# Performance work log

Hardware: AMD Instinct MI355X
Metric: run time of the kernel (lower is better)

## Reference

```python
import jax, jax.numpy as jnp
import numpy as np

B, T, D_IN = 256, 2048, 64
H1, H2, D_OUT = 256, 256, 2


def setup_inputs() -> dict:
    key = jax.random.key(0)
    ks = jax.random.split(key, 12)
    s = lambda fan_in: 1.0 / np.sqrt(fan_in)
    u = lambda k, shape, b: jax.random.uniform(k, shape, jnp.float32, -b, b)
    return {
        "input_tensor": jax.random.normal(ks[0], (B, T, D_IN), jnp.float32),
        # layer 0 LSTMCell params (torch layout: [4H, in], gate order i,f,g,o)
        "W_ih0": u(ks[1], (4 * H1, D_IN), s(H1)),
        "W_hh0": u(ks[2], (4 * H1, H1), s(H1)),
        "b_ih0": u(ks[3], (4 * H1,), s(H1)),
        "b_hh0": u(ks[4], (4 * H1,), s(H1)),
        # layer 1 LSTMCell params
        "W_ih1": u(ks[5], (4 * H2, H1), s(H2)),
        "W_hh1": u(ks[6], (4 * H2, H2), s(H2)),
        "b_ih1": u(ks[7], (4 * H2,), s(H2)),
        "b_hh1": u(ks[8], (4 * H2,), s(H2)),
        # dense head
        "W_dense": u(ks[9], (D_OUT, H2), s(H2)),
        "b_dense": u(ks[10], (D_OUT,), s(H2)),
    }


def _lstm_cell(x, h, c, W_ih, W_hh, b_ih, b_hh):
    # gates: [B, 4H]; torch gate order i, f, g, o
    g = x @ W_ih.T + h @ W_hh.T + (b_ih + b_hh)
    i, f, gg, o = jnp.split(g, 4, axis=-1)
    c_new = jax.nn.sigmoid(f) * c + jax.nn.sigmoid(i) * jnp.tanh(gg)
    h_new = jax.nn.sigmoid(o) * jnp.tanh(c_new)
    return h_new, c_new


def reference(input_tensor, W_ih0, W_hh0, b_ih0, b_hh0,
              W_ih1, W_hh1, b_ih1, b_hh1, W_dense, b_dense):
    b = input_tensor.shape[0]
    h0 = jnp.zeros((b, H1), input_tensor.dtype)
    c0 = jnp.zeros((b, H1), input_tensor.dtype)
    h1 = jnp.zeros((b, H2), input_tensor.dtype)
    c1 = jnp.zeros((b, H2), input_tensor.dtype)

    def step(carry, x_t):
        h0, c0, h1, c1 = carry
        h0, c0 = _lstm_cell(x_t, h0, c0, W_ih0, W_hh0, b_ih0, b_hh0)
        h1, c1 = _lstm_cell(h0, h1, c1, W_ih1, W_hh1, b_ih1, b_hh1)
        return (h0, c0, h1, c1), None

    xs = jnp.swapaxes(input_tensor, 0, 1)  # [T, B, D_IN]
    (h0, c0, h1, c1), _ = jax.lax.scan(step, (h0, c0, h1, c1), xs)
    # dropout_rate=0.0 -> identity; final_act_type='none' -> identity
    out = h1 @ W_dense.T + b_dense  # [B, D_OUT]
    return out
```

## Files before the change

### kernel.cpp

```cpp
#include <hip/hip_runtime.h>
#include <math.h>

#define TT 2048
#define DIN 64
#define HH 256
#define BR 32

typedef __attribute__((ext_vector_type(8))) short bf16x8;
typedef __attribute__((ext_vector_type(4))) float f32x4;
typedef unsigned short u16;

#define XS_STR 72
#define HS_STR 264
#define GB_STR 36

#define OFF_XS_HI  0
#define OFF_XS_LO  (OFF_XS_HI + 32*XS_STR)
#define OFF_HS0_HI (OFF_XS_LO + 32*XS_STR)
#define OFF_HS0_LO (OFF_HS0_HI + 32*HS_STR)
#define OFF_HS1_HI (OFF_HS0_LO + 32*HS_STR)
#define OFF_HS1_LO (OFF_HS1_HI + 32*HS_STR)
#define OFF_W0LO   (OFF_HS1_LO + 32*HS_STR)
#define OFF_W1LO   (OFF_W0LO + 1280*8)
#define SH_SHORTS  (OFF_W1LO + 2048*8)
#define SH_BYTES   (SH_SHORTS*2)
#define LDS_BYTES  (SH_BYTES + 2368*4)

__device__ __forceinline__ u16 f2bf(float f){
    unsigned u = __builtin_bit_cast(unsigned, f);
    u += 0x7fffu + ((u >> 16) & 1u);
    return (u16)(u >> 16);
}
__device__ __forceinline__ float bf2f(u16 h){
    unsigned u = ((unsigned)h) << 16;
    return __builtin_bit_cast(float, u);
}
__device__ __forceinline__ float sigf(float v){ return 1.0f/(1.0f+__expf(-v)); }

__device__ __forceinline__ void group_barrier(unsigned* cnt, unsigned target){
    __syncthreads();
    if (threadIdx.x == 0) {
        __hip_atomic_fetch_add(cnt, 1u, __ATOMIC_RELEASE, __HIP_MEMORY_SCOPE_AGENT);
        while (__hip_atomic_load(cnt, __ATOMIC_ACQUIRE, __HIP_MEMORY_SCOPE_AGENT) < target)
            __builtin_amdgcn_s_sleep(1);
    }
    __syncthreads();
}

__device__ __forceinline__ void split8(float4 a, float4 b, bf16x8& hi, bf16x8& lo){
    float v[8] = {a.x,a.y,a.z,a.w,b.x,b.y,b.z,b.w};
    #pragma unroll
    for (int j=0;j<8;++j){
        u16 h = f2bf(v[j]);
        hi[j] = (short)h;
        lo[j] = (short)f2bf(v[j] - bf2f(h));
    }
}

__global__ __launch_bounds__(256, 1)
void lstm_mfma(const float* __restrict__ x,
               const float* __restrict__ Wih0, const float* __restrict__ Whh0,
               const float* __restrict__ bih0, const float* __restrict__ bhh0,
               const float* __restrict__ Wih1, const float* __restrict__ Whh1,
               const float* __restrict__ bih1, const float* __restrict__ bhh1,
               const float* __restrict__ Wd,   const float* __restrict__ bd,
               float* __restrict__ out, u16* __restrict__ hb,
               unsigned* __restrict__ counters)
{
    extern __shared__ char smem[];
    short* sh  = (short*)smem;
    float* sf  = (float*)(smem + SH_BYTES);
    float* gb0 = sf;
    float* gb1 = sf + 1152;
    float* b0s = sf + 2304;
    float* b1s = sf + 2336;

    const int tid = threadIdx.x;
    const int w   = blockIdx.x;
    const int rb  = w & 7;
    const int ug  = w >> 3;
    const int rbase = rb * BR;
    const int u0  = ug * 8;

    unsigned* cnt = counters + rb * 64;


    const int l  = tid & 63;
    const int wv = tid >> 6;
    const int mt = wv >> 1, nt = wv & 1;
    const int c  = l & 15, ks = l >> 4;
    const int gbx = nt*2 + (c >> 3);
    const int g   = gbx*256 + u0 + (c & 7);

    bf16x8 w0h[10];
    #pragma unroll
    for (int kt = 0; kt < 10; ++kt) {
        int k = kt*32 + ks*8;
        const float* p = (k < 64) ? (Wih0 + (size_t)g*64 + k)
                                  : (Whh0 + (size_t)g*256 + (k - 64));
        bf16x8 hi_, lo_;
        split8(*(const float4*)p, *(const float4*)(p+4), hi_, lo_);
        w0h[kt] = hi_;
    }
    bf16x8 w1h[16];
    #pragma unroll
    for (int kt = 0; kt < 16; ++kt) {
        int k = kt*32 + ks*8;
        const float* p = (k < 256) ? (Wih1 + (size_t)g*256 + k)
                                   : (Whh1 + (size_t)g*256 + (k - 256));
        bf16x8 hi_, lo_;
        split8(*(const float4*)p, *(const float4*)(p+4), hi_, lo_);
        w1h[kt] = hi_;
    }
    for (int f = tid; f < 1280; f += 256) {
        int c_ = f & 15, ks_ = (f>>4)&3, nt_ = (f>>6)&1, kt_ = f>>7;
        int g_ = (nt_*2 + (c_>>3))*256 + u0 + (c_&7);
        int k_ = kt_*32 + ks_*8;
        const float* p = (k_ < 64) ? (Wih0 + (size_t)g_*64 + k_)
                                   : (Whh0 + (size_t)g_*256 + (k_ - 64));
        bf16x8 hi_, lo_;
        split8(*(const float4*)p, *(const float4*)(p+4), hi_, lo_);
        *(bf16x8*)(sh + OFF_W0LO + f*8) = lo_;
    }
    for (int f = tid; f < 2048; f += 256) {
        int c_ = f & 15, ks_ = (f>>4)&3, nt_ = (f>>6)&1, kt_ = f>>7;
        int g_ = (nt_*2 + (c_>>3))*256 + u0 + (c_&7);
        int k_ = kt_*32 + ks_*8;
        const float* p = (k_ < 256) ? (Wih1 + (size_t)g_*256 + k_)
                                    : (Whh1 + (size_t)g_*256 + (k_ - 256));
        bf16x8 hi_, lo_;
        split8(*(const float4*)p, *(const float4*)(p+4), hi_, lo_);
        *(bf16x8*)(sh + OFF_W1LO + f*8) = lo_;
    }

    if (tid < 32) {
        int gg_ = (tid >> 3)*256 + u0 + (tid & 7);
        b0s[tid] = bih0[gg_] + bhh0[gg_];
        b1s[tid] = bih1[gg_] + bhh1[gg_];
    }
    {
        int zr = tid >> 3, zu = tid & 7;
        size_t off = (size_t)(rbase + zr)*HH + u0 + zu;
        hb[off] = 0; hb[65536 + off] = 0;
        hb[131072 + off] = 0; hb[196608 + off] = 0;
        hb[262144 + off] = 0; hb[327680 + off] = 0;
        hb[393216 + off] = 0; hb[458752 + off] = 0;
    }
    {
        int xr = tid >> 3, xk = (tid & 7)*8;
        const float* xp = x + (size_t)(rbase + xr)*(TT*DIN) + xk;
        bf16x8 xh, xl;
        split8(*(const float4*)xp, *(const float4*)(xp+4), xh, xl);
        *(bf16x8*)(sh + OFF_XS_HI + xr*XS_STR + xk) = xh;
        *(bf16x8*)(sh + OFF_XS_LO + xr*XS_STR + xk) = xl;
    }
    unsigned epoch = 1;
    group_barrier(cnt, 32u*epoch);

    const int arow = mt*16 + c;
    const short* axh = sh + OFF_XS_HI  + arow*XS_STR + ks*8;
    const short* axl = sh + OFF_XS_LO  + arow*XS_STR + ks*8;
    const short* a0h = sh + OFF_HS0_HI + arow*HS_STR + ks*8;
    const short* a0l = sh + OFF_HS0_LO + arow*HS_STR + ks*8;
    const short* a1h = sh + OFF_HS1_HI + arow*HS_STR + ks*8;
    const short* a1l = sh + OFF_HS1_LO + arow*HS_STR + ks*8;
    const short* b0lo = sh + OFF_W0LO + (nt*64 + ks*16 + c)*8;
    const short* b1lo = sh + OFF_W1LO + (nt*64 + ks*16 + c)*8;
    float* gw0 = gb0 + (mt*16 + ks*4)*GB_STR + nt*16 + c;
    float* gw1 = gb1 + (mt*16 + ks*4)*GB_STR + nt*16 + c;
    const int ur = tid >> 3, uu = tid & 7;
    const size_t poff = (size_t)(rbase + ur)*HH + u0 + uu;

    float c0s = 0.f, c1s = 0.f;

    for (int k = 0; k <= TT; ++k) {
        {
            const unsigned rdo = ((k + 1) & 1) * 65536u;
            const u16* s0h = hb + rdo;
            const u16* s0l = hb + 131072 + rdo;
            const u16* s1h = hb + 262144 + rdo;
            const u16* s1l = hb + 393216 + rdo;
            #pragma unroll
            for (int j = 0; j < 4; ++j) {
                int cid = tid + j*256;
                int hr = cid >> 5, hk = (cid & 31)*8;
                size_t goff = (size_t)(rbase + hr)*HH + hk;
                int loff = hr*HS_STR + hk;
                *(uint4*)(sh + OFF_HS0_HI + loff) = *(const uint4*)(s0h + goff);
                *(uint4*)(sh + OFF_HS0_LO + loff) = *(const uint4*)(s0l + goff);
                *(uint4*)(sh + OFF_HS1_HI + loff) = *(const uint4*)(s1h + goff);
                *(uint4*)(sh + OFF_HS1_LO + loff) = *(const uint4*)(s1l + goff);
            }
        }
        __syncthreads();

        if (k < TT) {
            f32x4 ac[4] = {};
            #pragma unroll
            for (int kt = 0; kt < 10; ++kt) {
                const short* ph = (kt < 2) ? (axh + kt*32) : (a0h + (kt-2)*32);
                const short* pl = (kt < 2) ? (axl + kt*32) : (a0l + (kt-2)*32);
                bf16x8 ah = *(const bf16x8*)ph;
                bf16x8 al = *(const bf16x8*)pl;
                bf16x8 wl = *(const bf16x8*)(b0lo + kt*1024);
                const int q = kt & 3;
                ac[q] = __builtin_amdgcn_mfma_f32_16x16x32_bf16(ah, w0h[kt], ac[q], 0,0,0);
                ac[q] = __builtin_amdgcn_mfma_f32_16x16x32_bf16(al, w0h[kt], ac[q], 0,0,0);
                ac[q] = __builtin_amdgcn_mfma_f32_16x16x32_bf16(ah, wl,      ac[q], 0,0,0);
            }
            f32x4 aa = (ac[0] + ac[1]) + (ac[2] + ac[3]);
            gw0[0]        = aa[0];
            gw0[GB_STR]   = aa[1];
            gw0[2*GB_STR] = aa[2];
            gw0[3*GB_STR] = aa[3];
        }
        if (k >= 1) {
            f32x4 ac[4] = {};
            #pragma unroll
            for (int kt = 0; kt < 16; ++kt) {
                const short* ph = (kt < 8) ? (a0h + kt*32) : (a1h + (kt-8)*32);
                const short* pl = (kt < 8) ? (a0l + kt*32) : (a1l + (kt-8)*32);
                bf16x8 ah = *(const bf16x8*)ph;
                bf16x8 al = *(const bf16x8*)pl;
                bf16x8 wl = *(const bf16x8*)(b1lo + kt*1024);
                const int q = kt & 3;
                ac[q] = __builtin_amdgcn_mfma_f32_16x16x32_bf16(ah, w1h[kt], ac[q], 0,0,0);
                ac[q] = __builtin_amdgcn_mfma_f32_16x16x32_bf16(al, w1h[kt], ac[q], 0,0,0);
                ac[q] = __builtin_amdgcn_mfma_f32_16x16x32_bf16(ah, wl,      ac[q], 0,0,0);
            }
            f32x4 aa = (ac[0] + ac[1]) + (ac[2] + ac[3]);
            gw1[0]        = aa[0];
            gw1[GB_STR]   = aa[1];
            gw1[2*GB_STR] = aa[2];
            gw1[3*GB_STR] = aa[3];
        }
        __syncthreads();

        const unsigned wro = (k & 1) * 65536u;
        if (k < TT) {
            float gi = gb0[ur*GB_STR + uu]      + b0s[uu];
            float gf = gb0[ur*GB_STR + 8 + uu]  + b0s[8+uu];
            float gg = gb0[ur*GB_STR + 16 + uu] + b0s[16+uu];
            float go = gb0[ur*GB_STR + 24 + uu] + b0s[24+uu];
            c0s = sigf(gf)*c0s + sigf(gi)*tanhf(gg);
            float hn = sigf(go)*tanhf(c0s);
            u16 hh_ = f2bf(hn);
            u16 hl_ = f2bf(hn - bf2f(hh_));
            (hb + wro)[poff]          = hh_;
            (hb + 131072 + wro)[poff] = hl_;
        }
        if (k >= 1) {
            float gi = gb1[ur*GB_STR + uu]      + b1s[uu];
            float gf = gb1[ur*GB_STR + 8 + uu]  + b1s[8+uu];
            float gg = gb1[ur*GB_STR + 16 + uu] + b1s[16+uu];
            float go = gb1[ur*GB_STR + 24 + uu] + b1s[24+uu];
            c1s = sigf(gf)*c1s + sigf(gi)*tanhf(gg);
            float hn = sigf(go)*tanhf(c1s);
            u16 hh_ = f2bf(hn);
            u16 hl_ = f2bf(hn - bf2f(hh_));
            (hb + 262144 + wro)[poff] = hh_;
            (hb + 393216 + wro)[poff] = hl_;
        }
        if (k + 1 < TT) {
            int xr = tid >> 3, xk = (tid & 7)*8;
            const float* xp = x + (size_t)(rbase + xr)*(TT*DIN) + (size_t)(k+1)*DIN + xk;
            bf16x8 xh, xl;
            split8(*(const float4*)xp, *(const float4*)(xp+4), xh, xl);
            *(bf16x8*)(sh + OFF_XS_HI + xr*XS_STR + xk) = xh;
            *(bf16x8*)(sh + OFF_XS_LO + xr*XS_STR + xk) = xl;
        }
        ++epoch;
        group_barrier(cnt, 32u*epoch);
    }

    if (ug == 0 && tid < 64) {
        int r = tid >> 1, j = tid & 1;
        const u16* hhp = hb + 262144 + (size_t)(rbase + r)*HH;
        const u16* hlp = hb + 393216 + (size_t)(rbase + r)*HH;
        const float* wdp = Wd + j*HH;
        float a = bd[j];
        #pragma unroll 4
        for (int q = 0; q < HH; ++q)
            a += (bf2f(hhp[q]) + bf2f(hlp[q])) * wdp[q];
        out[(rbase + r)*2 + j] = a;
    }
}

extern "C" void kernel_launch(void* const* d_in, const int* in_sizes, int n_in,
                              void* d_out, int out_size, void* d_ws, size_t ws_size,
                              hipStream_t stream) {
    const float* x    = (const float*)d_in[0];
    const float* Wih0 = (const float*)d_in[1];
    const float* Whh0 = (const float*)d_in[2];
    const float* bih0 = (const float*)d_in[3];
    const float* bhh0 = (const float*)d_in[4];
    const float* Wih1 = (const float*)d_in[5];
    const float* Whh1 = (const float*)d_in[6];
    const float* bih1 = (const float*)d_in[7];
    const float* bhh1 = (const float*)d_in[8];
    const float* Wd   = (const float*)d_in[9];
    const float* bd   = (const float*)d_in[10];
    float* out = (float*)d_out;

    unsigned* counters = (unsigned*)d_ws;
    u16* hb = (u16*)((char*)d_ws + 4096);

    hipMemsetAsync(d_ws, 0, 4096, stream);

    hipFuncSetAttribute((const void*)lstm_mfma,
                        hipFuncAttributeMaxDynamicSharedMemorySize, LDS_BYTES);

    lstm_mfma<<<dim3(256), dim3(256), LDS_BYTES, stream>>>(
        x, Wih0, Whh0, bih0, bhh0, Wih1, Whh1, bih1, bhh1,
        Wd, bd, out, hb, counters);
}
```

Baseline: 16.18 ms.

## Split K across 8 waves with 32x32 MFMA and per-block flag barrier

Doubles the block to 512 threads and splits each step's GEMV along K across seven waves using 32x32x16 bf16 MFMAs, with partial gate sums combined by LDS atomicAdd. The cross-block barrier changes from a shared atomic counter to per-block epoch flags that 32 threads poll in parallel. The x tile is double-buffered, and the layer-0 and layer-1 cell updates now run concurrently on separate halves of the block. The aim is a shorter serial MFMA chain per step and cheaper synchronisation, in exchange for LDS atomics, extra zeroing of the gate buffers and higher register pressure.

```diff
diff --git a/kernel.cpp b/kernel.cpp
--- a/kernel.cpp
+++ b/kernel.cpp
@@ -7,24 +7,21 @@
 #define BR 32
 
 typedef __attribute__((ext_vector_type(8))) short bf16x8;
-typedef __attribute__((ext_vector_type(4))) float f32x4;
+typedef __attribute__((ext_vector_type(16))) float f32x16;
 typedef unsigned short u16;
 
 #define XS_STR 72
 #define HS_STR 264
 #define GB_STR 36
 
-#define OFF_XS_HI  0
-#define OFF_XS_LO  (OFF_XS_HI + 32*XS_STR)
-#define OFF_HS0_HI (OFF_XS_LO + 32*XS_STR)
-#define OFF_HS0_LO (OFF_HS0_HI + 32*HS_STR)
-#define OFF_HS1_HI (OFF_HS0_LO + 32*HS_STR)
-#define OFF_HS1_LO (OFF_HS1_HI + 32*HS_STR)
-#define OFF_W0LO   (OFF_HS1_LO + 32*HS_STR)
-#define OFF_W1LO   (OFF_W0LO + 1280*8)
-#define SH_SHORTS  (OFF_W1LO + 2048*8)
-#define SH_BYTES   (SH_SHORTS*2)
-#define LDS_BYTES  (SH_BYTES + 2368*4)
+#define OFF_XS    0
+#define OFF_HS0   9216
+#define OFF_HS1   26112
+#define OFF_W0LO  43008
+#define OFF_W1LO  53248
+#define SH_SHORTS 69632
+#define SH_BYTES  (SH_SHORTS*2)
+#define LDS_BYTES (SH_BYTES + 2368*4)
 
 __device__ __forceinline__ u16 f2bf(float f){
     unsigned u = __builtin_bit_cast(unsigned, f);
@@ -36,16 +33,6 @@
     return __builtin_bit_cast(float, u);
 }
 __device__ __forceinline__ float sigf(float v){ return 1.0f/(1.0f+__expf(-v)); }
-
-__device__ __forceinline__ void group_barrier(unsigned* cnt, unsigned target){
-    __syncthreads();
-    if (threadIdx.x == 0) {
-        __hip_atomic_fetch_add(cnt, 1u, __ATOMIC_RELEASE, __HIP_MEMORY_SCOPE_AGENT);
-        while (__hip_atomic_load(cnt, __ATOMIC_ACQUIRE, __HIP_MEMORY_SCOPE_AGENT) < target)
-            __builtin_amdgcn_s_sleep(1);
-    }
-    __syncthreads();
-}
 
 __device__ __forceinline__ void split8(float4 a, float4 b, bf16x8& hi, bf16x8& lo){
     float v[8] = {a.x,a.y,a.z,a.w,b.x,b.y,b.z,b.w};
@@ -57,18 +44,66 @@
     }
 }
 
-__global__ __launch_bounds__(256, 1)
-void lstm_mfma(const float* __restrict__ x,
-               const float* __restrict__ Wih0, const float* __restrict__ Whh0,
-               const float* __restrict__ bih0, const float* __restrict__ bhh0,
-               const float* __restrict__ Wih1, const float* __restrict__ Whh1,
-               const float* __restrict__ bih1, const float* __restrict__ bhh1,
-               const float* __restrict__ Wd,   const float* __restrict__ bd,
-               float* __restrict__ out, u16* __restrict__ hb,
-               unsigned* __restrict__ counters)
+__device__ __forceinline__ void group_barrier(unsigned* flg, int ug, unsigned epoch){
+    __syncthreads();
+    if (threadIdx.x == 0)
+        __hip_atomic_store(flg + ug*32, epoch, __ATOMIC_RELEASE, __HIP_MEMORY_SCOPE_AGENT);
+    if (threadIdx.x < 32) {
+        while (__hip_atomic_load(flg + threadIdx.x*32, __ATOMIC_ACQUIRE, __HIP_MEMORY_SCOPE_AGENT) < epoch)
+            __builtin_amdgcn_s_sleep(1);
+    }
+    __syncthreads();
+}
+
+template<int N>
+__device__ __forceinline__ void load_wh0(bf16x8* wh, int t0, int G, int hk8,
+                                         const float* Wih0, const float* Whh0){
+    #pragma unroll
+    for (int i=0;i<N;++i){
+        int k = (t0+i)*16 + hk8;
+        const float* p = (k < 64) ? (Wih0 + (size_t)G*64 + k) : (Whh0 + (size_t)G*HH + (k-64));
+        bf16x8 hi_, lo_; split8(*(const float4*)p, *(const float4*)(p+4), hi_, lo_);
+        wh[i] = hi_;
+    }
+}
+template<int N>
+__device__ __forceinline__ void load_wh1(bf16x8* wh, int t0, int G, int hk8,
+                                         const float* Wih1, const float* Whh1){
+    #pragma unroll
+    for (int i=0;i<N;++i){
+        int k = (t0+i)*16 + hk8;
+        const float* p = (k < 256) ? (Wih1 + (size_t)G*HH + k) : (Whh1 + (size_t)G*HH + (k-256));
+        bf16x8 hi_, lo_; split8(*(const float4*)p, *(const float4*)(p+4), hi_, lo_);
+        wh[i] = hi_;
+    }
+}
+
+template<int N>
+__device__ __forceinline__ void mm_run(const short* aHi, const short* aLo, const short* wlo,
+                                       const bf16x8* wh, f32x16* ac){
+    #pragma unroll
+    for (int i=0;i<N;++i){
+        bf16x8 ah = *(const bf16x8*)(aHi + i*16);
+        bf16x8 al = *(const bf16x8*)(aLo + i*16);
+        bf16x8 wl = *(const bf16x8*)(wlo + i*512);
+        ac[i&1] = __builtin_amdgcn_mfma_f32_32x32x16_bf16(ah, wh[i], ac[i&1], 0,0,0);
+        ac[i&1] = __builtin_amdgcn_mfma_f32_32x32x16_bf16(al, wh[i], ac[i&1], 0,0,0);
+        ac[i&1] = __builtin_amdgcn_mfma_f32_32x32x16_bf16(ah, wl,    ac[i&1], 0,0,0);
+    }
+}
+
+__global__ __launch_bounds__(512, 1)
+void lstm_mfma32(const float* __restrict__ x,
+                 const float* __restrict__ Wih0, const float* __restrict__ Whh0,
+                 const float* __restrict__ bih0, const float* __restrict__ bhh0,
+                 const float* __restrict__ Wih1, const float* __restrict__ Whh1,
+                 const float* __restrict__ bih1, const float* __restrict__ bhh1,
+                 const float* __restrict__ Wd,   const float* __restrict__ bd,
+                 float* __restrict__ out, u16* __restrict__ hb,
+                 unsigned* __restrict__ flags)
 {
     extern __shared__ char smem[];
-    short* sh  = (short*)smem;
+    short* sh = (short*)smem;
     float* sf  = (float*)(smem + SH_BYTES);
     float* gb0 = sf;
     float* gb1 = sf + 1152;
@@ -81,208 +116,182 @@
     const int ug  = w >> 3;
     const int rbase = rb * BR;
     const int u0  = ug * 8;
-
-    unsigned* cnt = counters + rb * 64;
-
-
-    const int l  = tid & 63;
-    const int wv = tid >> 6;
-    const int mt = wv >> 1, nt = wv & 1;
-    const int c  = l & 15, ks = l >> 4;
-    const int gbx = nt*2 + (c >> 3);
-    const int g   = gbx*256 + u0 + (c & 7);
-
-    bf16x8 w0h[10];
-    #pragma unroll
-    for (int kt = 0; kt < 10; ++kt) {
-        int k = kt*32 + ks*8;
-        const float* p = (k < 64) ? (Wih0 + (size_t)g*64 + k)
-                                  : (Whh0 + (size_t)g*256 + (k - 64));
-        bf16x8 hi_, lo_;
-        split8(*(const float4*)p, *(const float4*)(p+4), hi_, lo_);
-        w0h[kt] = hi_;
-    }
-    bf16x8 w1h[16];
-    #pragma unroll
-    for (int kt = 0; kt < 16; ++kt) {
-        int k = kt*32 + ks*8;
-        const float* p = (k < 256) ? (Wih1 + (size_t)g*256 + k)
-                                   : (Whh1 + (size_t)g*256 + (k - 256));
-        bf16x8 hi_, lo_;
-        split8(*(const float4*)p, *(const float4*)(p+4), hi_, lo_);
-        w1h[kt] = hi_;
-    }
-    for (int f = tid; f < 1280; f += 256) {
-        int c_ = f & 15, ks_ = (f>>4)&3, nt_ = (f>>6)&1, kt_ = f>>7;
-        int g_ = (nt_*2 + (c_>>3))*256 + u0 + (c_&7);
-        int k_ = kt_*32 + ks_*8;
-        const float* p = (k_ < 64) ? (Wih0 + (size_t)g_*64 + k_)
-                                   : (Whh0 + (size_t)g_*256 + (k_ - 64));
-        bf16x8 hi_, lo_;
-        split8(*(const float4*)p, *(const float4*)(p+4), hi_, lo_);
+    unsigned* flg = flags + rb * 1024;
+
+
+    const int l   = tid & 63;
+    const int wid = tid >> 6;
+    const int col = l & 31;
+    const int kg  = l >> 5;
+    const int hk8 = kg * 8;
+    const int row = col;
+
+    const int G = (col>>3)*HH + u0 + (col&7);
+
+    bf16x8 wh[8];
+    if      (wid==0) load_wh0<7>(wh, 0,  G, hk8, Wih0, Whh0);
+    else if (wid==1) load_wh0<7>(wh, 7,  G, hk8, Wih0, Whh0);
+    else if (wid==2) load_wh0<6>(wh, 14, G, hk8, Wih0, Whh0);
+    else if (wid==3) load_wh1<8>(wh, 0,  G, hk8, Wih1, Whh1);
+    else if (wid==4) load_wh1<8>(wh, 8,  G, hk8, Wih1, Whh1);
+    else if (wid==5) load_wh1<8>(wh, 16, G, hk8, Wih1, Whh1);
+    else if (wid==6) load_wh1<8>(wh, 24, G, hk8, Wih1, Whh1);
+
+    for (int f = tid; f < 20*64; f += 512){
+        int kt = f >> 6, ll = f & 63;
+        int c2 = ll & 31;
+        int G2 = (c2>>3)*HH + u0 + (c2&7);
+        int k  = kt*16 + (ll>>5)*8;
+        const float* p = (k<64) ? (Wih0 + (size_t)G2*64 + k) : (Whh0 + (size_t)G2*HH + (k-64));
+        bf16x8 hi_, lo_; split8(*(const float4*)p, *(const float4*)(p+4), hi_, lo_);
         *(bf16x8*)(sh + OFF_W0LO + f*8) = lo_;
     }
-    for (int f = tid; f < 2048; f += 256) {
-        int c_ = f & 15, ks_ = (f>>4)&3, nt_ = (f>>6)&1, kt_ = f>>7;
-        int g_ = (nt_*2 + (c_>>3))*256 + u0 + (c_&7);
-        int k_ = kt_*32 + ks_*8;
-        const float* p = (k_ < 256) ? (Wih1 + (size_t)g_*256 + k_)
-                                    : (Whh1 + (size_t)g_*256 + (k_ - 256));
-        bf16x8 hi_, lo_;
-        split8(*(const float4*)p, *(const float4*)(p+4), hi_, lo_);
+    for (int f = tid; f < 32*64; f += 512){
+        int kt = f >> 6, ll = f & 63;
+        int c2 = ll & 31;
+        int G2 = (c2>>3)*HH + u0 + (c2&7);
+        int k  = kt*16 + (ll>>5)*8;
+        const float* p = (k<256) ? (Wih1 + (size_t)G2*HH + k) : (Whh1 + (size_t)G2*HH + (k-256));
+        bf16x8 hi_, lo_; split8(*(const float4*)p, *(const float4*)(p+4), hi_, lo_);
         *(bf16x8*)(sh + OFF_W1LO + f*8) = lo_;
     }
 
-    if (tid < 32) {
-        int gg_ = (tid >> 3)*256 + u0 + (tid & 7);
+    if (tid < 32){
+        int gg_ = (tid>>3)*HH + u0 + (tid&7);
         b0s[tid] = bih0[gg_] + bhh0[gg_];
         b1s[tid] = bih1[gg_] + bhh1[gg_];
     }
-    {
-        int zr = tid >> 3, zu = tid & 7;
-        size_t off = (size_t)(rbase + zr)*HH + u0 + zu;
-        hb[off] = 0; hb[65536 + off] = 0;
-        hb[131072 + off] = 0; hb[196608 + off] = 0;
-        hb[262144 + off] = 0; hb[327680 + off] = 0;
-        hb[393216 + off] = 0; hb[458752 + off] = 0;
-    }
-    {
-        int xr = tid >> 3, xk = (tid & 7)*8;
-        const float* xp = x + (size_t)(rbase + xr)*(TT*DIN) + xk;
-        bf16x8 xh, xl;
-        split8(*(const float4*)xp, *(const float4*)(xp+4), xh, xl);
-        *(bf16x8*)(sh + OFF_XS_HI + xr*XS_STR + xk) = xh;
-        *(bf16x8*)(sh + OFF_XS_LO + xr*XS_STR + xk) = xl;
-    }
-    unsigned epoch = 1;
-    group_barrier(cnt, 32u*epoch);
-
-    const int arow = mt*16 + c;
-    const short* axh = sh + OFF_XS_HI  + arow*XS_STR + ks*8;
-    const short* axl = sh + OFF_XS_LO  + arow*XS_STR + ks*8;
-    const short* a0h = sh + OFF_HS0_HI + arow*HS_STR + ks*8;
-    const short* a0l = sh + OFF_HS0_LO + arow*HS_STR + ks*8;
-    const short* a1h = sh + OFF_HS1_HI + arow*HS_STR + ks*8;
-    const short* a1l = sh + OFF_HS1_LO + arow*HS_STR + ks*8;
-    const short* b0lo = sh + OFF_W0LO + (nt*64 + ks*16 + c)*8;
-    const short* b1lo = sh + OFF_W1LO + (nt*64 + ks*16 + c)*8;
-    float* gw0 = gb0 + (mt*16 + ks*4)*GB_STR + nt*16 + c;
-    float* gw1 = gb1 + (mt*16 + ks*4)*GB_STR + nt*16 + c;
-    const int ur = tid >> 3, uu = tid & 7;
-    const size_t poff = (size_t)(rbase + ur)*HH + u0 + uu;
+    if (tid < 256){
+        int zr = tid>>3, zu = tid&7;
+        size_t off = (size_t)(rbase+zr)*HH + u0 + zu;
+        hb[off]=0; hb[65536+off]=0; hb[131072+off]=0; hb[196608+off]=0;
+        hb[262144+off]=0; hb[327680+off]=0; hb[393216+off]=0; hb[458752+off]=0;
+    } else {
+        int lo_ = tid-256;
+        int xr = lo_>>3, xk = (lo_&7)*8;
+        const float* xp = x + (size_t)(rbase+xr)*(TT*DIN) + xk;
+        bf16x8 xh, xl; split8(*(const float4*)xp, *(const float4*)(xp+4), xh, xl);
+        *(bf16x8*)(sh + OFF_XS + xr*XS_STR + xk) = xh;
+        *(bf16x8*)(sh + OFF_XS + 2304 + xr*XS_STR + xk) = xl;
+    }
+    group_barrier(flg, ug, 1u);
+
+    const short* a0h = sh + OFF_HS0 +        row*HS_STR + hk8;
+    const short* a0l = sh + OFF_HS0 + 8448 + row*HS_STR + hk8;
+    const short* a1h = sh + OFF_HS1 +        row*HS_STR + hk8;
+    const short* a1l = sh + OFF_HS1 + 8448 + row*HS_STR + hk8;
+    const short* wlo0 = sh + OFF_W0LO + l*8;
+    const short* wlo1 = sh + OFF_W1LO + l*8;
+
+    const int upd = (tid < 256) ? tid : (tid - 256);
+    const int ur = upd >> 3, uu = upd & 7;
+    const size_t poff = (size_t)(rbase+ur)*HH + u0 + uu;
 
     float c0s = 0.f, c1s = 0.f;
 
-    for (int k = 0; k <= TT; ++k) {
+    for (int k = 0; k <= TT; ++k){
         {
-            const unsigned rdo = ((k + 1) & 1) * 65536u;
-            const u16* s0h = hb + rdo;
-            const u16* s0l = hb + 131072 + rdo;
-            const u16* s1h = hb + 262144 + rdo;
-            const u16* s1l = hb + 393216 + rdo;
+            const unsigned rdo = ((k+1)&1) * 65536u;
             #pragma unroll
-            for (int j = 0; j < 4; ++j) {
-                int cid = tid + j*256;
-                int hr = cid >> 5, hk = (cid & 31)*8;
-                size_t goff = (size_t)(rbase + hr)*HH + hk;
-                int loff = hr*HS_STR + hk;
-                *(uint4*)(sh + OFF_HS0_HI + loff) = *(const uint4*)(s0h + goff);
-                *(uint4*)(sh + OFF_HS0_LO + loff) = *(const uint4*)(s0l + goff);
-                *(uint4*)(sh + OFF_HS1_HI + loff) = *(const uint4*)(s1h + goff);
-                *(uint4*)(sh + OFF_HS1_LO + loff) = *(const uint4*)(s1l + goff);
-            }
+            for (int j=0;j<8;++j){
+                int cid = tid + j*512;
+                int p = cid >> 10, u = cid & 1023;
+                int hr = u >> 5, hk = (u&31)*8;
+                *(uint4*)(sh + OFF_HS0 + p*8448 + hr*HS_STR + hk) =
+                    *(const uint4*)(hb + (size_t)p*131072 + rdo + (size_t)(rbase+hr)*HH + hk);
+            }
+            float4 z = {0.f,0.f,0.f,0.f};
+            for (int i4 = tid; i4 < 576; i4 += 512) *(float4*)(sf + i4*4) = z;
         }
         __syncthreads();
 
-        if (k < TT) {
-            f32x4 ac[4] = {};
-            #pragma unroll
-            for (int kt = 0; kt < 10; ++kt) {
-                const short* ph = (kt < 2) ? (axh + kt*32) : (a0h + (kt-2)*32);
-                const short* pl = (kt < 2) ? (axl + kt*32) : (a0l + (kt-2)*32);
-                bf16x8 ah = *(const bf16x8*)ph;
-                bf16x8 al = *(const bf16x8*)pl;
-                bf16x8 wl = *(const bf16x8*)(b0lo + kt*1024);
-                const int q = kt & 3;
-                ac[q] = __builtin_amdgcn_mfma_f32_16x16x32_bf16(ah, w0h[kt], ac[q], 0,0,0);
-                ac[q] = __builtin_amdgcn_mfma_f32_16x16x32_bf16(al, w0h[kt], ac[q], 0,0,0);
-                ac[q] = __builtin_amdgcn_mfma_f32_16x16x32_bf16(ah, wl,      ac[q], 0,0,0);
-            }
-            f32x4 aa = (ac[0] + ac[1]) + (ac[2] + ac[3]);
-            gw0[0]        = aa[0];
-            gw0[GB_STR]   = aa[1];
-            gw0[2*GB_STR] = aa[2];
-            gw0[3*GB_STR] = aa[3];
-        }
-        if (k >= 1) {
-            f32x4 ac[4] = {};
-            #pragma unroll
-            for (int kt = 0; kt < 16; ++kt) {
-                const short* ph = (kt < 8) ? (a0h + kt*32) : (a1h + (kt-8)*32);
-                const short* pl = (kt < 8) ? (a0l + kt*32) : (a1l + (kt-8)*32);
-                bf16x8 ah = *(const bf16x8*)ph;
-                bf16x8 al = *(const bf16x8*)pl;
-                bf16x8 wl = *(const bf16x8*)(b1lo + kt*1024);
-                const int q = kt & 3;
-                ac[q] = __builtin_amdgcn_mfma_f32_16x16x32_bf16(ah, w1h[kt], ac[q], 0,0,0);
-                ac[q] = __builtin_amdgcn_mfma_f32_16x16x32_bf16(al, w1h[kt], ac[q], 0,0,0);
-                ac[q] = __builtin_amdgcn_mfma_f32_16x16x32_bf16(ah, wl,      ac[q], 0,0,0);
-            }
-            f32x4 aa = (ac[0] + ac[1]) + (ac[2] + ac[3]);
-            gw1[0]        = aa[0];
-            gw1[GB_STR]   = aa[1];
-            gw1[2*GB_STR] = aa[2];
-            gw1[3*GB_STR] = aa[3];
+        if (wid < 3){
+            if (k < TT){
+                f32x16 ac[2] = {};
+                if (wid==0){
+                    const short* xh = sh + OFF_XS + (k&1)*4608 +        row*XS_STR + hk8;
+                    const short* xl = sh + OFF_XS + (k&1)*4608 + 2304 + row*XS_STR + hk8;
+                    mm_run<4>(xh, xl, wlo0, wh, ac);
+                    mm_run<3>(a0h, a0l, wlo0 + 4*512, wh+4, ac);
+                } else if (wid==1){
+                    mm_run<7>(a0h + 3*16, a0l + 3*16, wlo0 + 7*512, wh, ac);
+                } else {
+                    mm_run<6>(a0h + 10*16, a0l + 10*16, wlo0 + 14*512, wh, ac);
+                }
+                f32x16 aa = ac[0] + ac[1];
+                float* gp = gb0 + col;
+                #pragma unroll
+                for (int r2=0;r2<16;++r2){
+                    int rr = (r2&3) + ((r2>>2)<<3) + (kg<<2);
+                    atomicAdd(gp + rr*GB_STR, aa[r2]);
+                }
+            }
+        } else if (wid < 7){
+            if (k >= 1){
+                f32x16 ac[2] = {};
+                if      (wid==3) mm_run<8>(a0h,          a0l,          wlo1,          wh, ac);
+                else if (wid==4) mm_run<8>(a0h + 8*16,   a0l + 8*16,   wlo1 + 8*512,  wh, ac);
+                else if (wid==5) mm_run<8>(a1h,          a1l,          wlo1 + 16*512, wh, ac);
+                else             mm_run<8>(a1h + 8*16,   a1l + 8*16,   wlo1 + 24*512, wh, ac);
+                f32x16 aa = ac[0] + ac[1];
+                float* gp = gb1 + col;
+                #pragma unroll
+                for (int r2=0;r2<16;++r2){
+                    int rr = (r2&3) + ((r2>>2)<<3) + (kg<<2);
+                    atomicAdd(gp + rr*GB_STR, aa[r2]);
+                }
+            }
         }
         __syncthreads();
 
-        const unsigned wro = (k & 1) * 65536u;
-        if (k < TT) {
-            float gi = gb0[ur*GB_STR + uu]      + b0s[uu];
-            float gf = gb0[ur*GB_STR + 8 + uu]  + b0s[8+uu];
-            float gg = gb0[ur*GB_STR + 16 + uu] + b0s[16+uu];
-            float go = gb0[ur*GB_STR + 24 + uu] + b0s[24+uu];
-            c0s = sigf(gf)*c0s + sigf(gi)*tanhf(gg);
-            float hn = sigf(go)*tanhf(c0s);
-            u16 hh_ = f2bf(hn);
-            u16 hl_ = f2bf(hn - bf2f(hh_));
-            (hb + wro)[poff]          = hh_;
-            (hb + 131072 + wro)[poff] = hl_;
+        const unsigned wro = (k&1) * 65536u;
+        if (tid < 256){
+            if (k < TT){
+                float gi = gb0[ur*GB_STR + uu]      + b0s[uu];
+                float gf = gb0[ur*GB_STR + 8 + uu]  + b0s[8+uu];
+                float gg = gb0[ur*GB_STR + 16 + uu] + b0s[16+uu];
+                float go = gb0[ur*GB_STR + 24 + uu] + b0s[24+uu];
+                c0s = sigf(gf)*c0s + sigf(gi)*tanhf(gg);
+                float hn = sigf(go)*tanhf(c0s);
+                u16 hhv = f2bf(hn), hlv = f2bf(hn - bf2f(hhv));
+                hb[wro + poff]          = hhv;
+                hb[131072 + wro + poff] = hlv;
+            }
+        } else {
+            if (k >= 1){
+                float gi = gb1[ur*GB_STR + uu]      + b1s[uu];
+                float gf = gb1[ur*GB_STR + 8 + uu]  + b1s[8+uu];
+                float gg = gb1[ur*GB_STR + 16 + uu] + b1s[16+uu];
+                float go = gb1[ur*GB_STR + 24 + uu] + b1s[24+uu];
+                c1s = sigf(gf)*c1s + sigf(gi)*tanhf(gg);
+                float hn = sigf(go)*tanhf(c1s);
+                u16 hhv = f2bf(hn), hlv = f2bf(hn - bf2f(hhv));
+                hb[262144 + wro + poff] = hhv;
+                hb[393216 + wro + poff] = hlv;
+            }
+            if (k + 1 < TT){
+                int lo_ = tid-256;
+                int xr = lo_>>3, xk = (lo_&7)*8;
+                const float* xp = x + (size_t)(rbase+xr)*(TT*DIN) + (size_t)(k+1)*DIN + xk;
+                bf16x8 xh, xl; split8(*(const float4*)xp, *(const float4*)(xp+4), xh, xl);
+                int pb = ((k+1)&1)*4608;
+                *(bf16x8*)(sh + OFF_XS + pb +        xr*XS_STR + xk) = xh;
+                *(bf16x8*)(sh + OFF_XS + pb + 2304 + xr*XS_STR + xk) = xl;
+            }
         }
-        if (k >= 1) {
-            float gi = gb1[ur*GB_STR + uu]      + b1s[uu];
-            float gf = gb1[ur*GB_STR + 8 + uu]  + b1s[8+uu];
-            float gg = gb1[ur*GB_STR + 16 + uu] + b1s[16+uu];
-            float go = gb1[ur*GB_STR + 24 + uu] + b1s[24+uu];
-            c1s = sigf(gf)*c1s + sigf(gi)*tanhf(gg);
-            float hn = sigf(go)*tanhf(c1s);
-            u16 hh_ = f2bf(hn);
-            u16 hl_ = f2bf(hn - bf2f(hh_));
-            (hb + 262144 + wro)[poff] = hh_;
-            (hb + 393216 + wro)[poff] = hl_;
-        }
-        if (k + 1 < TT) {
-            int xr = tid >> 3, xk = (tid & 7)*8;
-            const float* xp = x + (size_t)(rbase + xr)*(TT*DIN) + (size_t)(k+1)*DIN + xk;
-            bf16x8 xh, xl;
-            split8(*(const float4*)xp, *(const float4*)(xp+4), xh, xl);
-            *(bf16x8*)(sh + OFF_XS_HI + xr*XS_STR + xk) = xh;
-            *(bf16x8*)(sh + OFF_XS_LO + xr*XS_STR + xk) = xl;
-        }
-        ++epoch;
-        group_barrier(cnt, 32u*epoch);
-    }
-
-    if (ug == 0 && tid < 64) {
+        group_barrier(flg, ug, (unsigned)(k+2));
+    }
+
+    if (ug == 0 && tid < 64){
         int r = tid >> 1, j = tid & 1;
-        const u16* hhp = hb + 262144 + (size_t)(rbase + r)*HH;
-        const u16* hlp = hb + 393216 + (size_t)(rbase + r)*HH;
+        const u16* hhp = hb + 262144 + (size_t)(rbase+r)*HH;
+        const u16* hlp = hb + 393216 + (size_t)(rbase+r)*HH;
         const float* wdp = Wd + j*HH;
         float a = bd[j];
         #pragma unroll 4
         for (int q = 0; q < HH; ++q)
             a += (bf2f(hhp[q]) + bf2f(hlp[q])) * wdp[q];
-        out[(rbase + r)*2 + j] = a;
+        out[(rbase+r)*2 + j] = a;
     }
 }
 
@@ -302,15 +311,15 @@
     const float* bd   = (const float*)d_in[10];
     float* out = (float*)d_out;
 
-    unsigned* counters = (unsigned*)d_ws;
-    u16* hb = (u16*)((char*)d_ws + 4096);
-
-    hipMemsetAsync(d_ws, 0, 4096, stream);
-
-    hipFuncSetAttribute((const void*)lstm_mfma,
+    unsigned* flags = (unsigned*)d_ws;
+    u16* hb = (u16*)((char*)d_ws + 32768);
+
+    hipMemsetAsync(d_ws, 0, 32768, stream);
+
+    hipFuncSetAttribute((const void*)lstm_mfma32,
                         hipFuncAttributeMaxDynamicSharedMemorySize, LDS_BYTES);
 
-    lstm_mfma<<<dim3(256), dim3(256), LDS_BYTES, stream>>>(
+    lstm_mfma32<<<dim3(256), dim3(512), LDS_BYTES, stream>>>(
         x, Wih0, Whh0, bih0, bhh0, Wih1, Whh1, bih1, bhh1,
-        Wd, bd, out, hb, counters);
-}
+        Wd, bd, out, hb, flags);
+}
```

Result: slower. 35.84 ms (+121.6%).

## Use per-block flag barrier, fragment-ordered LDS layout, and double-buffered x tile

Applied to the files above, without the earlier changes.

The single shared atomic counter in the inter-block group barrier is replaced with per-block epoch flags on separate cache lines, polled in parallel by 32 lanes, so arrivals no longer contend on one atomic. The h-state and x tiles in LDS are stored in MFMA fragment order, so each lane reads a contiguous bf16x8 and padded strides are no longer needed. The x tile is double-buffered by step parity. The aim is to cut barrier latency on the serial time loop and avoid LDS bank conflicts, at the cost of a larger flag workspace and more polling traffic.

```diff
diff --git a/kernel.cpp b/kernel.cpp
--- a/kernel.cpp
+++ b/kernel.cpp
@@ -4,48 +4,32 @@
 #define TT 2048
 #define DIN 64
 #define HH 256
-#define BR 32
 
 typedef __attribute__((ext_vector_type(8))) short bf16x8;
 typedef __attribute__((ext_vector_type(4))) float f32x4;
+typedef unsigned u32t;
 typedef unsigned short u16;
 
-#define XS_STR 72
-#define HS_STR 264
+#define OFF_XS    0
+#define OFF_H0    8192
+#define OFF_H1    24576
+#define OFF_W0LO  40960
+#define OFF_W1LO  51200
+#define SH_SHORTS 67584
+#define SH_BYTES  (SH_SHORTS*2)
 #define GB_STR 36
-
-#define OFF_XS_HI  0
-#define OFF_XS_LO  (OFF_XS_HI + 32*XS_STR)
-#define OFF_HS0_HI (OFF_XS_LO + 32*XS_STR)
-#define OFF_HS0_LO (OFF_HS0_HI + 32*HS_STR)
-#define OFF_HS1_HI (OFF_HS0_LO + 32*HS_STR)
-#define OFF_HS1_LO (OFF_HS1_HI + 32*HS_STR)
-#define OFF_W0LO   (OFF_HS1_LO + 32*HS_STR)
-#define OFF_W1LO   (OFF_W0LO + 1280*8)
-#define SH_SHORTS  (OFF_W1LO + 2048*8)
-#define SH_BYTES   (SH_SHORTS*2)
-#define LDS_BYTES  (SH_BYTES + 2368*4)
+#define LDS_BYTES (SH_BYTES + 2368*4)
 
 __device__ __forceinline__ u16 f2bf(float f){
-    unsigned u = __builtin_bit_cast(unsigned, f);
+    u32t u = __builtin_bit_cast(u32t, f);
     u += 0x7fffu + ((u >> 16) & 1u);
     return (u16)(u >> 16);
 }
 __device__ __forceinline__ float bf2f(u16 h){
-    unsigned u = ((unsigned)h) << 16;
+    u32t u = ((u32t)h) << 16;
     return __builtin_bit_cast(float, u);
 }
 __device__ __forceinline__ float sigf(float v){ return 1.0f/(1.0f+__expf(-v)); }
-
-__device__ __forceinline__ void group_barrier(unsigned* cnt, unsigned target){
-    __syncthreads();
-    if (threadIdx.x == 0) {
-        __hip_atomic_fetch_add(cnt, 1u, __ATOMIC_RELEASE, __HIP_MEMORY_SCOPE_AGENT);
-        while (__hip_atomic_load(cnt, __ATOMIC_ACQUIRE, __HIP_MEMORY_SCOPE_AGENT) < target)
-            __builtin_amdgcn_s_sleep(1);
-    }
-    __syncthreads();
-}
 
 __device__ __forceinline__ void split8(float4 a, float4 b, bf16x8& hi, bf16x8& lo){
     float v[8] = {a.x,a.y,a.z,a.w,b.x,b.y,b.z,b.w};
@@ -57,15 +41,28 @@
     }
 }
 
+__device__ __forceinline__ void group_barrier(u32t* flg, int ug, unsigned epoch){
+    __syncthreads();
+    if (threadIdx.x == 0)
+        __hip_atomic_store(flg + ug*16, epoch, __ATOMIC_RELEASE, __HIP_MEMORY_SCOPE_AGENT);
+    if (threadIdx.x < 32) {
+        while (__hip_atomic_load(flg + threadIdx.x*16, __ATOMIC_ACQUIRE, __HIP_MEMORY_SCOPE_AGENT) < epoch)
+            __builtin_amdgcn_s_sleep(1);
+    }
+    __syncthreads();
+}
+
+#define MFMA16(a,b,c_) __builtin_amdgcn_mfma_f32_16x16x32_bf16(a,b,c_,0,0,0)
+
 __global__ __launch_bounds__(256, 1)
-void lstm_mfma(const float* __restrict__ x,
-               const float* __restrict__ Wih0, const float* __restrict__ Whh0,
-               const float* __restrict__ bih0, const float* __restrict__ bhh0,
-               const float* __restrict__ Wih1, const float* __restrict__ Whh1,
-               const float* __restrict__ bih1, const float* __restrict__ bhh1,
-               const float* __restrict__ Wd,   const float* __restrict__ bd,
-               float* __restrict__ out, u16* __restrict__ hb,
-               unsigned* __restrict__ counters)
+void lstm_v7(const float* __restrict__ x,
+             const float* __restrict__ Wih0, const float* __restrict__ Whh0,
+             const float* __restrict__ bih0, const float* __restrict__ bhh0,
+             const float* __restrict__ Wih1, const float* __restrict__ Whh1,
+             const float* __restrict__ bih1, const float* __restrict__ bhh1,
+             const float* __restrict__ Wd,   const float* __restrict__ bd,
+             float* __restrict__ out, u16* __restrict__ hb,
+             u32t* __restrict__ flags)
 {
     extern __shared__ char smem[];
     short* sh  = (short*)smem;
@@ -79,10 +76,10 @@
     const int w   = blockIdx.x;
     const int rb  = w & 7;
     const int ug  = w >> 3;
-    const int rbase = rb * BR;
+    const int rbase = rb * 32;
     const int u0  = ug * 8;
 
-    unsigned* cnt = counters + rb * 64;
+    u32t* flg = flags + rb * 512;
 
 
     const int l  = tid & 63;
@@ -90,14 +87,14 @@
     const int mt = wv >> 1, nt = wv & 1;
     const int c  = l & 15, ks = l >> 4;
     const int gbx = nt*2 + (c >> 3);
-    const int g   = gbx*256 + u0 + (c & 7);
+    const int g   = gbx*HH + u0 + (c & 7);
 
     bf16x8 w0h[10];
     #pragma unroll
     for (int kt = 0; kt < 10; ++kt) {
         int k = kt*32 + ks*8;
         const float* p = (k < 64) ? (Wih0 + (size_t)g*64 + k)
-                                  : (Whh0 + (size_t)g*256 + (k - 64));
+                                  : (Whh0 + (size_t)g*HH + (k - 64));
         bf16x8 hi_, lo_;
         split8(*(const float4*)p, *(const float4*)(p+4), hi_, lo_);
         w0h[kt] = hi_;
@@ -106,35 +103,35 @@
     #pragma unroll
     for (int kt = 0; kt < 16; ++kt) {
         int k = kt*32 + ks*8;
-        const float* p = (k < 256) ? (Wih1 + (size_t)g*256 + k)
-                                   : (Whh1 + (size_t)g*256 + (k - 256));
+        const float* p = (k < 256) ? (Wih1 + (size_t)g*HH + k)
+                                   : (Whh1 + (size_t)g*HH + (k - 256));
         bf16x8 hi_, lo_;
         split8(*(const float4*)p, *(const float4*)(p+4), hi_, lo_);
         w1h[kt] = hi_;
     }
     for (int f = tid; f < 1280; f += 256) {
         int c_ = f & 15, ks_ = (f>>4)&3, nt_ = (f>>6)&1, kt_ = f>>7;
-        int g_ = (nt_*2 + (c_>>3))*256 + u0 + (c_&7);
+        int g_ = (nt_*2 + (c_>>3))*HH + u0 + (c_&7);
         int k_ = kt_*32 + ks_*8;
         const float* p = (k_ < 64) ? (Wih0 + (size_t)g_*64 + k_)
-                                   : (Whh0 + (size_t)g_*256 + (k_ - 64));
+                                   : (Whh0 + (size_t)g_*HH + (k_ - 64));
         bf16x8 hi_, lo_;
         split8(*(const float4*)p, *(const float4*)(p+4), hi_, lo_);
         *(bf16x8*)(sh + OFF_W0LO + f*8) = lo_;
     }
     for (int f = tid; f < 2048; f += 256) {
         int c_ = f & 15, ks_ = (f>>4)&3, nt_ = (f>>6)&1, kt_ = f>>7;
-        int g_ = (nt_*2 + (c_>>3))*256 + u0 + (c_&7);
+        int g_ = (nt_*2 + (c_>>3))*HH + u0 + (c_&7);
         int k_ = kt_*32 + ks_*8;
-        const float* p = (k_ < 256) ? (Wih1 + (size_t)g_*256 + k_)
-                                    : (Whh1 + (size_t)g_*256 + (k_ - 256));
+        const float* p = (k_ < 256) ? (Wih1 + (size_t)g_*HH + k_)
+                                    : (Whh1 + (size_t)g_*HH + (k_ - 256));
         bf16x8 hi_, lo_;
         split8(*(const float4*)p, *(const float4*)(p+4), hi_, lo_);
         *(bf16x8*)(sh + OFF_W1LO + f*8) = lo_;
     }
 
     if (tid < 32) {
-        int gg_ = (tid >> 3)*256 + u0 + (tid & 7);
+        int gg_ = (tid >> 3)*HH + u0 + (tid & 7);
         b0s[tid] = bih0[gg_] + bhh0[gg_];
         b1s[tid] = bih1[gg_] + bhh1[gg_];
     }
@@ -147,23 +144,18 @@
         hb[393216 + off] = 0; hb[458752 + off] = 0;
     }
     {
-        int xr = tid >> 3, xk = (tid & 7)*8;
-        const float* xp = x + (size_t)(rbase + xr)*(TT*DIN) + xk;
+        int r = tid & 31, c8 = tid >> 5;
+        const float* xp = x + (size_t)(rbase + r)*(TT*DIN) + c8*8;
         bf16x8 xh, xl;
         split8(*(const float4*)xp, *(const float4*)(xp+4), xh, xl);
-        *(bf16x8*)(sh + OFF_XS_HI + xr*XS_STR + xk) = xh;
-        *(bf16x8*)(sh + OFF_XS_LO + xr*XS_STR + xk) = xl;
-    }
-    unsigned epoch = 1;
-    group_barrier(cnt, 32u*epoch);
-
-    const int arow = mt*16 + c;
-    const short* axh = sh + OFF_XS_HI  + arow*XS_STR + ks*8;
-    const short* axl = sh + OFF_XS_LO  + arow*XS_STR + ks*8;
-    const short* a0h = sh + OFF_HS0_HI + arow*HS_STR + ks*8;
-    const short* a0l = sh + OFF_HS0_LO + arow*HS_STR + ks*8;
-    const short* a1h = sh + OFF_HS1_HI + arow*HS_STR + ks*8;
-    const short* a1l = sh + OFF_HS1_LO + arow*HS_STR + ks*8;
+        int fo = ((c8>>2)*2 + (r>>4))*512 + ((c8&3)*16 + (r&15))*8;
+        *(bf16x8*)(sh + OFF_XS + fo)        = xh;
+        *(bf16x8*)(sh + OFF_XS + 2048 + fo) = xl;
+    }
+    group_barrier(flg, ug, 1u);
+
+    const short* h0A = sh + OFF_H0 + mt*512 + l*8;
+    const short* h1A = sh + OFF_H1 + mt*512 + l*8;
     const short* b0lo = sh + OFF_W0LO + (nt*64 + ks*16 + c)*8;
     const short* b1lo = sh + OFF_W1LO + (nt*64 + ks*16 + c)*8;
     float* gw0 = gb0 + (mt*16 + ks*4)*GB_STR + nt*16 + c;
@@ -176,37 +168,34 @@
     for (int k = 0; k <= TT; ++k) {
         {
             const unsigned rdo = ((k + 1) & 1) * 65536u;
-            const u16* s0h = hb + rdo;
-            const u16* s0l = hb + 131072 + rdo;
-            const u16* s1h = hb + 262144 + rdo;
-            const u16* s1l = hb + 393216 + rdo;
             #pragma unroll
             for (int j = 0; j < 4; ++j) {
-                int cid = tid + j*256;
-                int hr = cid >> 5, hk = (cid & 31)*8;
-                size_t goff = (size_t)(rbase + hr)*HH + hk;
-                int loff = hr*HS_STR + hk;
-                *(uint4*)(sh + OFF_HS0_HI + loff) = *(const uint4*)(s0h + goff);
-                *(uint4*)(sh + OFF_HS0_LO + loff) = *(const uint4*)(s0l + goff);
-                *(uint4*)(sh + OFF_HS1_HI + loff) = *(const uint4*)(s1h + goff);
-                *(uint4*)(sh + OFF_HS1_LO + loff) = *(const uint4*)(s1l + goff);
+                int idx = tid + j*256;
+                int r = idx & 31, c8 = idx >> 5;
+                size_t goff = (size_t)(rbase + r)*HH + c8*8;
+                int fo = ((c8>>2)*2 + (r>>4))*512 + ((c8&3)*16 + (r&15))*8;
+                *(uint4*)(sh + OFF_H0 + fo)         = *(const uint4*)(hb + rdo + goff);
+                *(uint4*)(sh + OFF_H0 + 8192 + fo)  = *(const uint4*)(hb + 131072 + rdo + goff);
+                *(uint4*)(sh + OFF_H1 + fo)         = *(const uint4*)(hb + 262144 + rdo + goff);
+                *(uint4*)(sh + OFF_H1 + 8192 + fo)  = *(const uint4*)(hb + 393216 + rdo + goff);
             }
         }
         __syncthreads();
 
         if (k < TT) {
+            const short* xA = sh + OFF_XS + (k&1)*4096 + mt*512 + l*8;
             f32x4 ac[4] = {};
             #pragma unroll
             for (int kt = 0; kt < 10; ++kt) {
-                const short* ph = (kt < 2) ? (axh + kt*32) : (a0h + (kt-2)*32);
-                const short* pl = (kt < 2) ? (axl + kt*32) : (a0l + (kt-2)*32);
+                const short* ph = (kt < 2) ? (xA + kt*1024) : (h0A + (kt-2)*1024);
+                const short* pl = ph + ((kt < 2) ? 2048 : 8192);
                 bf16x8 ah = *(const bf16x8*)ph;
                 bf16x8 al = *(const bf16x8*)pl;
                 bf16x8 wl = *(const bf16x8*)(b0lo + kt*1024);
                 const int q = kt & 3;
-                ac[q] = __builtin_amdgcn_mfma_f32_16x16x32_bf16(ah, w0h[kt], ac[q], 0,0,0);
-                ac[q] = __builtin_amdgcn_mfma_f32_16x16x32_bf16(al, w0h[kt], ac[q], 0,0,0);
-                ac[q] = __builtin_amdgcn_mfma_f32_16x16x32_bf16(ah, wl,      ac[q], 0,0,0);
+                ac[q] = MFMA16(ah, w0h[kt], ac[q]);
+                ac[q] = MFMA16(al, w0h[kt], ac[q]);
+                ac[q] = MFMA16(ah, wl,      ac[q]);
             }
             f32x4 aa = (ac[0] + ac[1]) + (ac[2] + ac[3]);
             gw0[0]        = aa[0];
@@ -218,15 +207,15 @@
             f32x4 ac[4] = {};
             #pragma unroll
             for (int kt = 0; kt < 16; ++kt) {
-                const short* ph = (kt < 8) ? (a0h + kt*32) : (a1h + (kt-8)*32);
-                const short* pl = (kt < 8) ? (a0l + kt*32) : (a1l + (kt-8)*32);
+                const short* ph = (kt < 8) ? (h0A + kt*1024) : (h1A + (kt-8)*1024);
+                const short* pl = ph + 8192;
                 bf16x8 ah = *(const bf16x8*)ph;
                 bf16x8 al = *(const bf16x8*)pl;
                 bf16x8 wl = *(const bf16x8*)(b1lo + kt*1024);
                 const int q = kt & 3;
-                ac[q] = __builtin_amdgcn_mfma_f32_16x16x32_bf16(ah, w1h[kt], ac[q], 0,0,0);
-                ac[q] = __builtin_amdgcn_mfma_f32_16x16x32_bf16(al, w1h[kt], ac[q], 0,0,0);
-                ac[q] = __builtin_amdgcn_mfma_f32_16x16x32_bf16(ah, wl,      ac[q], 0,0,0);
+                ac[q] = MFMA16(ah, w1h[kt], ac[q]);
+                ac[q] = MFMA16(al, w1h[kt], ac[q]);
+                ac[q] = MFMA16(ah, wl,      ac[q]);
             }
             f32x4 aa = (ac[0] + ac[1]) + (ac[2] + ac[3]);
             gw1[0]        = aa[0];
@@ -262,15 +251,16 @@
             (hb + 393216 + wro)[poff] = hl_;
         }
         if (k + 1 < TT) {
-            int xr = tid >> 3, xk = (tid & 7)*8;
-            const float* xp = x + (size_t)(rbase + xr)*(TT*DIN) + (size_t)(k+1)*DIN + xk;
+            int r = tid & 31, c8 = tid >> 5;
+            const float* xp = x + (size_t)(rbase + r)*(TT*DIN) + (size_t)(k+1)*DIN + c8*8;
             bf16x8 xh, xl;
             split8(*(const float4*)xp, *(const float4*)(xp+4), xh, xl);
-            *(bf16x8*)(sh + OFF_XS_HI + xr*XS_STR + xk) = xh;
-            *(bf16x8*)(sh + OFF_XS_LO + xr*XS_STR + xk) = xl;
-        }
-        ++epoch;
-        group_barrier(cnt, 32u*epoch);
+            int pb = ((k+1)&1)*4096;
+            int fo = ((c8>>2)*2 + (r>>4))*512 + ((c8&3)*16 + (r&15))*8;
+            *(bf16x8*)(sh + OFF_XS + pb + fo)        = xh;
+            *(bf16x8*)(sh + OFF_XS + pb + 2048 + fo) = xl;
+        }
+        group_barrier(flg, ug, (unsigned)(k+2));
     }
 
     if (ug == 0 && tid < 64) {
@@ -302,15 +292,15 @@
     const float* bd   = (const float*)d_in[10];
     float* out = (float*)d_out;
 
-    unsigned* counters = (unsigned*)d_ws;
-    u16* hb = (u16*)((char*)d_ws + 4096);
-
-    hipMemsetAsync(d_ws, 0, 4096, stream);
-
-    hipFuncSetAttribute((const void*)lstm_mfma,
+    u32t* flags = (u32t*)d_ws;
+    u16* hb = (u16*)((char*)d_ws + 32768);
+
+    hipMemsetAsync(d_ws, 0, 32768, stream);
+
+    hipFuncSetAttribute((const void*)lstm_v7,
                         hipFuncAttributeMaxDynamicSharedMemorySize, LDS_BYTES);
 
-    lstm_mfma<<<dim3(256), dim3(256), LDS_BYTES, stream>>>(
+    lstm_v7<<<dim3(256), dim3(256), LDS_BYTES, stream>>>(
         x, Wih0, Whh0, bih0, bhh0, Wih1, Whh1, bih1, bhh1,
-        Wd, bd, out, hb, counters);
-}
+        Wd, bd, out, hb, flags);
+}
```

Result: slower. 23.07 ms (+42.6%).
